# Kernel optimization log

Hardware: AMD Instinct MI355X
Metric: run time of the kernel (lower is better)

The kernel has to match this reference:

```python
import jax, jax.numpy as jnp
import numpy as np
from jax.scipy.linalg import expm

B, NUM_WS, Z_DIM, MAT_DIM = 4096, 16, 512, 10
INIT_SCALE = 0.001


def setup_inputs() -> dict:
    key = jax.random.key(0)
    k1, k2 = jax.random.split(key)
    z = jax.random.normal(k1, (B, NUM_WS, Z_DIM), dtype=jnp.float32)
    # learned Lie-algebra basis, initialized N(0, init_scale) as in the module
    lie_alg_basis = jax.random.normal(k2, (NUM_WS, Z_DIM, MAT_DIM, MAT_DIM), dtype=jnp.float32) * INIT_SCALE
    return {"z": z, "lie_alg_basis": lie_alg_basis}


def reference(z, lie_alg_basis):
    # weighted sum of basis matrices per (batch, ws): [b, w, m, m]
    lie_alg = jnp.einsum('bwz,wzij->bwij', z, lie_alg_basis)
    b, w, m, _ = lie_alg.shape
    # batched small matrix exponential over b*w tiny (m x m) matrices
    lie_group = jax.vmap(expm)(lie_alg.reshape(b * w, m, m))
    return lie_group.reshape(b, w, m, m)
```

## Files before the change

### kernel.cpp

```cpp
#include <hip/hip_runtime.h>
#include <hip/hip_bf16.h>

#define NWS 16
#define ZD 512
#define MM 100
#define NCOL 112
#define HALF_BYTES 57344
#define PANEL_BYTES 114688

typedef __attribute__((ext_vector_type(8))) short bf16x8;
typedef __attribute__((ext_vector_type(4))) float f32x4;

static __device__ __forceinline__ unsigned short f2bf(float x) {
    union { __hip_bfloat16 h; unsigned short u; } cv;
    cv.h = __float2bfloat16(x);
    return cv.u;
}

__global__ __launch_bounds__(256) void prep_basis(const float* __restrict__ basis,
                                                  unsigned char* __restrict__ Bt) {
    const int idx = blockIdx.x * 256 + threadIdx.x;
    const int col  = idx % NCOL;
    const int rest = idx / NCOL;
    const int g    = rest & 63;
    const int w    = rest >> 6;

    bf16x8 pk;
    #pragma unroll
    for (int e = 0; e < 8; ++e) {
        const int k = g * 8 + e;
        const float v = (col < MM) ? basis[((size_t)(w * ZD + k)) * MM + col] : 0.f;
        pk[e] = (short)f2bf(v);
    }
    const int half = g >> 5;
    const int gl   = g & 31;
    const size_t off = (size_t)w * PANEL_BYTES + (size_t)half * HALF_BYTES
                     + (size_t)col * 512 + (size_t)((gl * 16) ^ ((col & 7) << 4));
    *reinterpret_cast<bf16x8*>(Bt + off) = pk;
}

__global__ __launch_bounds__(512, 4) void einsum_mfma(const float* __restrict__ z,
                                                      const unsigned char* __restrict__ Btg,
                                                      float* __restrict__ out) {
    __shared__ __align__(16) unsigned char Bs[HALF_BYTES];
    const int w     = blockIdx.x;
    const int chunk = blockIdx.y;
    const int tid   = threadIdx.x;
    const int wave  = tid >> 6;
    const int lane  = tid & 63;
    const int l15   = lane & 15;
    const int k8    = lane >> 4;

    const int row = chunk * 128 + wave * 16 + l15;
    const float* zp = z + (size_t)row * (NWS * ZD) + (size_t)w * ZD + k8 * 8;
    const unsigned char* bt = Btg + (size_t)w * PANEL_BYTES;

    int bbase[7];
    #pragma unroll
    for (int nf = 0; nf < 7; ++nf) bbase[nf] = (nf * 16 + l15) * 512;
    const int bswz = (l15 & 7) << 4;

    f32x4 acc[7];
    #pragma unroll
    for (int nf = 0; nf < 7; ++nf) acc[nf] = (f32x4){0.f, 0.f, 0.f, 0.f};

    float4 za[2][2];
    za[0][0] = *reinterpret_cast<const float4*>(zp);
    za[0][1] = *reinterpret_cast<const float4*>(zp + 4);

    #pragma unroll
    for (int half = 0; half < 2; ++half) {
        if (half) __syncthreads();
        float4 st[7];
        const float4* gsrc = reinterpret_cast<const float4*>(bt + half * HALF_BYTES);
        #pragma unroll
        for (int i = 0; i < 7; ++i) st[i] = gsrc[i * 512 + tid];
        #pragma unroll
        for (int i = 0; i < 7; ++i)
            *reinterpret_cast<float4*>(Bs + i * 8192 + tid * 16) = st[i];
        __syncthreads();

        #pragma unroll
        for (int step = 0; step < 8; ++step) {
            const int gs  = half * 8 + step;
            const int cur = step & 1;
            const int nxt = cur ^ 1;
            if (gs < 15) {
                za[nxt][0] = *reinterpret_cast<const float4*>(zp + (gs + 1) * 32);
                za[nxt][1] = *reinterpret_cast<const float4*>(zp + (gs + 1) * 32 + 4);
            }
            bf16x8 af;
            af[0] = (short)f2bf(za[cur][0].x);
            af[1] = (short)f2bf(za[cur][0].y);
            af[2] = (short)f2bf(za[cur][0].z);
            af[3] = (short)f2bf(za[cur][0].w);
            af[4] = (short)f2bf(za[cur][1].x);
            af[5] = (short)f2bf(za[cur][1].y);
            af[6] = (short)f2bf(za[cur][1].z);
            af[7] = (short)f2bf(za[cur][1].w);

            const int klb = (step * 64 + k8 * 16) ^ bswz;
            #pragma unroll
            for (int nf = 0; nf < 7; ++nf) {
                const bf16x8 bfr = *reinterpret_cast<const bf16x8*>(Bs + bbase[nf] + klb);
                acc[nf] = __builtin_amdgcn_mfma_f32_16x16x32_bf16(af, bfr, acc[nf], 0, 0, 0);
            }
        }
    }

    const int rowbase = chunk * 128 + wave * 16 + k8 * 4;
    #pragma unroll
    for (int nf = 0; nf < 7; ++nf) {
        const int col = nf * 16 + l15;
        if (col < MM) {
            #pragma unroll
            for (int r = 0; r < 4; ++r)
                out[((size_t)(rowbase + r) * NWS + w) * MM + col] = acc[nf][r];
        }
    }
}

#define EXP_NT 6

__global__ __launch_bounds__(320, 2) void expm_kernel(float* __restrict__ out) {
    __shared__ float As[64 * 100];
    const int t = threadIdx.x;
    const size_t base = (size_t)blockIdx.x * 6400;

    #pragma unroll
    for (int q = 0; q < 5; ++q) {
        const int idx = (q * 320 + t) * 4;
        *reinterpret_cast<float4*>(&As[idx]) =
            *reinterpret_cast<const float4*>(out + base + idx);
    }
    __syncthreads();

    const int m  = t / 5;
    const int c  = t - m * 5;
    const int j0 = 2 * c, j1 = j0 + 1;
    const float* A = &As[m * 100];

    float a[100];
    #pragma unroll
    for (int q = 0; q < 25; ++q) {
        const float4 v = *reinterpret_cast<const float4*>(A + q * 4);
        a[q * 4 + 0] = v.x; a[q * 4 + 1] = v.y;
        a[q * 4 + 2] = v.z; a[q * 4 + 3] = v.w;
    }

    float p0[10], p1[10];
    #pragma unroll
    for (int i = 0; i < 10; ++i) {
        p0[i] = A[i * 10 + j0] * (1.f / EXP_NT) + ((i == j0) ? 1.f : 0.f);
        p1[i] = A[i * 10 + j1] * (1.f / EXP_NT) + ((i == j1) ? 1.f : 0.f);
    }

    #pragma unroll
    for (int k = EXP_NT - 1; k >= 1; --k) {
        float n0[10], n1[10];
        #pragma unroll
        for (int i = 0; i < 10; ++i) { n0[i] = 0.f; n1[i] = 0.f; }
        #pragma unroll
        for (int kk = 0; kk < 10; ++kk) {
            const float q0 = p0[kk], q1 = p1[kk];
            #pragma unroll
            for (int i = 0; i < 10; ++i) {
                n0[i] = fmaf(a[i * 10 + kk], q0, n0[i]);
                n1[i] = fmaf(a[i * 10 + kk], q1, n1[i]);
            }
        }
        const float invk = 1.f / (float)k;
        #pragma unroll
        for (int i = 0; i < 10; ++i) {
            p0[i] = n0[i] * invk + ((i == j0) ? 1.f : 0.f);
            p1[i] = n1[i] * invk + ((i == j1) ? 1.f : 0.f);
        }
    }

    #pragma unroll
    for (int i = 0; i < 10; ++i)
        *reinterpret_cast<float2*>(out + base + m * 100 + i * 10 + j0) =
            make_float2(p0[i], p1[i]);
}

extern "C" void kernel_launch(void* const* d_in, const int* in_sizes, int n_in,
                              void* d_out, int out_size, void* d_ws, size_t ws_size,
                              hipStream_t stream) {
    const float* z     = (const float*)d_in[0];
    const float* basis = (const float*)d_in[1];
    float* out = (float*)d_out;
    unsigned char* Bt = (unsigned char*)d_ws;

    prep_basis<<<(NWS * 64 * NCOL) / 256, 256, 0, stream>>>(basis, Bt);

    dim3 gridA(NWS, 32);
    einsum_mfma<<<gridA, 512, 0, stream>>>(z, Bt, out);

    expm_kernel<<<(4096 * NWS) / 64, 320, 0, stream>>>(out);
}
```

Baseline: 56.28 us.

## Double-buffer basis panel in quarters via direct global-to-LDS loads

Splits the per-ws basis panel into four K-quarters and double-buffers them in LDS, loading each next quarter with global_load_lds while MFMAs consume the current one. It also prefetches a whole quarter of z values at once instead of one step ahead. The aim is to overlap basis staging with compute and drop the register round trip for LDS fills. Shared memory per block stays the same (two quarter buffers), but register use for z prefetch grows and the global_load_lds path depends on the per-lane LDS addressing matching the layout.

```diff
diff --git a/kernel.cpp b/kernel.cpp
--- a/kernel.cpp
+++ b/kernel.cpp
@@ -5,7 +5,7 @@
 #define ZD 512
 #define MM 100
 #define NCOL 112
-#define HALF_BYTES 57344
+#define QBYTES 28672
 #define PANEL_BYTES 114688
 
 typedef __attribute__((ext_vector_type(8))) short bf16x8;
@@ -32,17 +32,17 @@
         const float v = (col < MM) ? basis[((size_t)(w * ZD + k)) * MM + col] : 0.f;
         pk[e] = (short)f2bf(v);
     }
-    const int half = g >> 5;
-    const int gl   = g & 31;
-    const size_t off = (size_t)w * PANEL_BYTES + (size_t)half * HALF_BYTES
-                     + (size_t)col * 512 + (size_t)((gl * 16) ^ ((col & 7) << 4));
+    const int q  = g >> 4;
+    const int gl = g & 15;
+    const size_t off = (size_t)w * PANEL_BYTES + (size_t)q * QBYTES
+                     + (size_t)col * 256 + (size_t)((gl * 16) ^ ((col & 7) << 4));
     *reinterpret_cast<bf16x8*>(Bt + off) = pk;
 }
 
 __global__ __launch_bounds__(512, 4) void einsum_mfma(const float* __restrict__ z,
                                                       const unsigned char* __restrict__ Btg,
                                                       float* __restrict__ out) {
-    __shared__ __align__(16) unsigned char Bs[HALF_BYTES];
+    __shared__ __align__(16) unsigned char Bs[2][QBYTES];
     const int w     = blockIdx.x;
     const int chunk = blockIdx.y;
     const int tid   = threadIdx.x;
@@ -57,55 +57,74 @@
 
     int bbase[7];
     #pragma unroll
-    for (int nf = 0; nf < 7; ++nf) bbase[nf] = (nf * 16 + l15) * 512;
+    for (int nf = 0; nf < 7; ++nf) bbase[nf] = (nf * 16 + l15) * 256;
     const int bswz = (l15 & 7) << 4;
 
+    float4 zf[8];
+
+    #define STAGE_Q(t, buf)                                                              \
+        do {                                                                             \
+            const unsigned char* gq = bt + (t) * QBYTES;                                 \
+            _Pragma("unroll")                                                            \
+            for (int r = 0; r < 3; ++r) {                                                \
+                __builtin_amdgcn_global_load_lds(                                        \
+                    (const __attribute__((address_space(1))) unsigned int*)(gq + (r * 512 + tid) * 16), \
+                    (__attribute__((address_space(3))) unsigned int*)(&Bs[buf][(r * 512 + tid) * 16]),  \
+                    16, 0, 0);                                                           \
+            }                                                                            \
+            if (tid < 256) {                                                             \
+                __builtin_amdgcn_global_load_lds(                                        \
+                    (const __attribute__((address_space(1))) unsigned int*)(gq + (1536 + tid) * 16),    \
+                    (__attribute__((address_space(3))) unsigned int*)(&Bs[buf][(1536 + tid) * 16]),     \
+                    16, 0, 0);                                                           \
+            }                                                                            \
+        } while (0)
+
+    #define ZLOAD_Q(t)                                                                   \
+        do {                                                                             \
+            _Pragma("unroll")                                                            \
+            for (int j = 0; j < 4; ++j) {                                                \
+                zf[2 * j]     = *reinterpret_cast<const float4*>(zp + ((t) * 4 + j) * 32);      \
+                zf[2 * j + 1] = *reinterpret_cast<const float4*>(zp + ((t) * 4 + j) * 32 + 4);  \
+            }                                                                            \
+        } while (0)
+
     f32x4 acc[7];
     #pragma unroll
     for (int nf = 0; nf < 7; ++nf) acc[nf] = (f32x4){0.f, 0.f, 0.f, 0.f};
 
-    float4 za[2][2];
-    za[0][0] = *reinterpret_cast<const float4*>(zp);
-    za[0][1] = *reinterpret_cast<const float4*>(zp + 4);
-
-    #pragma unroll
-    for (int half = 0; half < 2; ++half) {
-        if (half) __syncthreads();
-        float4 st[7];
-        const float4* gsrc = reinterpret_cast<const float4*>(bt + half * HALF_BYTES);
-        #pragma unroll
-        for (int i = 0; i < 7; ++i) st[i] = gsrc[i * 512 + tid];
-        #pragma unroll
-        for (int i = 0; i < 7; ++i)
-            *reinterpret_cast<float4*>(Bs + i * 8192 + tid * 16) = st[i];
-        __syncthreads();
-
-        #pragma unroll
-        for (int step = 0; step < 8; ++step) {
-            const int gs  = half * 8 + step;
-            const int cur = step & 1;
-            const int nxt = cur ^ 1;
-            if (gs < 15) {
-                za[nxt][0] = *reinterpret_cast<const float4*>(zp + (gs + 1) * 32);
-                za[nxt][1] = *reinterpret_cast<const float4*>(zp + (gs + 1) * 32 + 4);
-            }
-            bf16x8 af;
-            af[0] = (short)f2bf(za[cur][0].x);
-            af[1] = (short)f2bf(za[cur][0].y);
-            af[2] = (short)f2bf(za[cur][0].z);
-            af[3] = (short)f2bf(za[cur][0].w);
-            af[4] = (short)f2bf(za[cur][1].x);
-            af[5] = (short)f2bf(za[cur][1].y);
-            af[6] = (short)f2bf(za[cur][1].z);
-            af[7] = (short)f2bf(za[cur][1].w);
-
-            const int klb = (step * 64 + k8 * 16) ^ bswz;
+    STAGE_Q(0, 0);
+    ZLOAD_Q(0);
+    __syncthreads();
+
+    #pragma unroll
+    for (int t = 0; t < 4; ++t) {
+        bf16x8 zb[4];
+        #pragma unroll
+        for (int j = 0; j < 4; ++j) {
+            zb[j][0] = (short)f2bf(zf[2 * j].x);
+            zb[j][1] = (short)f2bf(zf[2 * j].y);
+            zb[j][2] = (short)f2bf(zf[2 * j].z);
+            zb[j][3] = (short)f2bf(zf[2 * j].w);
+            zb[j][4] = (short)f2bf(zf[2 * j + 1].x);
+            zb[j][5] = (short)f2bf(zf[2 * j + 1].y);
+            zb[j][6] = (short)f2bf(zf[2 * j + 1].z);
+            zb[j][7] = (short)f2bf(zf[2 * j + 1].w);
+        }
+        if (t < 3) {
+            STAGE_Q(t + 1, (t + 1) & 1);
+            ZLOAD_Q(t + 1);
+        }
+        #pragma unroll
+        for (int s = 0; s < 4; ++s) {
+            const int klb = (s * 64 + k8 * 16) ^ bswz;
             #pragma unroll
             for (int nf = 0; nf < 7; ++nf) {
-                const bf16x8 bfr = *reinterpret_cast<const bf16x8*>(Bs + bbase[nf] + klb);
-                acc[nf] = __builtin_amdgcn_mfma_f32_16x16x32_bf16(af, bfr, acc[nf], 0, 0, 0);
+                const bf16x8 bfr = *reinterpret_cast<const bf16x8*>(&Bs[t & 1][bbase[nf] + klb]);
+                acc[nf] = __builtin_amdgcn_mfma_f32_16x16x32_bf16(zb[s], bfr, acc[nf], 0, 0, 0);
             }
         }
+        if (t < 3) __syncthreads();
     }
 
     const int rowbase = chunk * 128 + wave * 16 + k8 * 4;
@@ -118,6 +137,8 @@
                 out[((size_t)(rowbase + r) * NWS + w) * MM + col] = acc[nf][r];
         }
     }
+    #undef STAGE_Q
+    #undef ZLOAD_Q
 }
 
 #define EXP_NT 6
```

Result: slower. 58.34 us (+3.7%).
